# Kernel tuning notes

Hardware: AMD Instinct MI355X
Metric: run time of the kernel (lower is better)

Reference implementation:

```python
import jax, jax.numpy as jnp
import numpy as np

D_MODEL = 768
N_HEAD = 12
HEAD_DIM = D_MODEL // N_HEAD
D_FF = 4 * D_MODEL
EPS = 1e-5


def setup_inputs() -> dict:
    key = jax.random.key(0)
    ks = jax.random.split(key, 12)
    B, S = 4, 1024
    s = 0.02
    return {
        "x": jax.random.normal(ks[0], (B, S, D_MODEL), jnp.float32),
        "ln1_g": jnp.ones((D_MODEL,), jnp.float32),
        "ln1_b": jnp.zeros((D_MODEL,), jnp.float32),
        "ln2_g": jnp.ones((D_MODEL,), jnp.float32),
        "ln2_b": jnp.zeros((D_MODEL,), jnp.float32),
        "w_attn": jax.random.normal(ks[1], (D_MODEL, 3 * D_MODEL), jnp.float32) * s,
        "b_attn": jnp.zeros((3 * D_MODEL,), jnp.float32),
        "w_proj": jax.random.normal(ks[2], (D_MODEL, D_MODEL), jnp.float32) * s,
        "b_proj": jnp.zeros((D_MODEL,), jnp.float32),
        "w_fc": jax.random.normal(ks[3], (D_MODEL, D_FF), jnp.float32) * s,
        "b_fc": jnp.zeros((D_FF,), jnp.float32),
        "w_mlp_proj": jax.random.normal(ks[4], (D_FF, D_MODEL), jnp.float32) * s,
        "b_mlp_proj": jnpp.zeros((D_MODEL,), jnp.float32) if False else jnp.zeros((D_MODEL,), jnp.float32),
    }


def layer_norm(x, g, b):
    mu = jnp.mean(x, axis=-1, keepdims=True)
    var = jnp.mean(jnp.square(x - mu), axis=-1, keepdims=True)
    return (x - mu) * jax.lax.rsqrt(var + EPS) * g + b


def attention(x, w_attn, b_attn, w_proj, b_proj):
    B, S, _ = x.shape
    qkv = x @ w_attn + b_attn                      # [B,S,3D]
    q, k, v = jnp.split(qkv, 3, axis=-1)
    def heads(t):
        return t.reshape(B, S, N_HEAD, HEAD_DIM).transpose(0, 2, 1, 3)  # [B,H,S,hd]
    q, k, v = heads(q), heads(k), heads(v)
    scale = HEAD_DIM ** (-0.5)
    att = jnp.einsum("bhqd,bhkd->bhqk", q, k) * scale
    # additive causal mask: strictly-upper triangle gets -1e9 (matches TF source)
    mask = 1.0 - jnp.tril(jnp.ones((S, S), att.dtype))
    att = att + mask * (-1e9)
    att = jax.nn.softmax(att, axis=-1)
    y = jnp.einsum("bhqk,bhkd->bhqd", att, v)
    y = y.transpose(0, 2, 1, 3).reshape(B, S, D_MODEL)
    return y @ w_proj + b_proj


def mlp(x, w_fc, b_fc, w_mlp_proj, b_mlp_proj):
    h = jax.nn.gelu(x @ w_fc + b_fc, approximate=True)
    return h @ w_mlp_proj + b_mlp_proj


def reference(x, ln1_g, ln1_b, ln2_g, ln2_b, w_attn, b_attn, w_proj, b_proj,
              w_fc, b_fc, w_mlp_proj, b_mlp_proj):
    x = x + attention(layer_norm(x, ln1_g, ln1_b), w_attn, b_attn, w_proj, b_proj)
    x = x + mlp(layer_norm(x, ln2_g, ln2_b), w_fc, b_fc, w_mlp_proj, b_mlp_proj)
    return x
```

## Files before the change

### kernel.cpp

```cpp
#include <hip/hip_runtime.h>

typedef unsigned short u16;
typedef short bf8_t __attribute__((ext_vector_type(8)));
typedef float f32x4 __attribute__((ext_vector_type(4)));

__device__ __forceinline__ u16 f2bf(float f) {
  unsigned u = __builtin_bit_cast(unsigned, f);
  unsigned r = (u + 0x7fffu + ((u >> 16) & 1u)) >> 16;
  return (u16)r;
}

__device__ __forceinline__ void gld16(const void* g, void* l) {
  __builtin_amdgcn_global_load_lds((const __attribute__((address_space(1))) unsigned int*)g,
                                   (__attribute__((address_space(3))) unsigned int*)l, 16, 0, 0);
}

#define MFMA(a, b, c) __builtin_amdgcn_mfma_f32_16x16x32_bf16((a), (b), (c), 0, 0, 0)

__global__ void wtrans_kernel(const float* __restrict__ W, u16* __restrict__ WT, int K, int N) {
  __shared__ float tile[32][33];
  const int n0 = blockIdx.x << 5, k0 = blockIdx.y << 5;
  const int tx = threadIdx.x, ty = threadIdx.y;
#pragma unroll
  for (int i = 0; i < 4; i++) {
    const int r = ty + (i << 3);
    tile[r][tx] = W[(size_t)(k0 + r) * N + n0 + tx];
  }
  __syncthreads();
#pragma unroll
  for (int i = 0; i < 4; i++) {
    const int r = ty + (i << 3);
    WT[(size_t)(n0 + r) * K + k0 + tx] = f2bf(tile[tx][r]);
  }
}

__global__ void ln_kernel(const float* __restrict__ x, const float* __restrict__ g,
                          const float* __restrict__ bb, u16* __restrict__ o) {
  const int row = blockIdx.x, t = threadIdx.x;
  const float* xr = x + (size_t)row * 768;
  float v[3];
#pragma unroll
  for (int i = 0; i < 3; i++) v[i] = xr[t + (i << 8)];
  float s = v[0] + v[1] + v[2];
#pragma unroll
  for (int off = 1; off < 64; off <<= 1) s += __shfl_xor(s, off, 64);
  __shared__ float red[4];
  const int w = t >> 6;
  if ((t & 63) == 0) red[w] = s;
  __syncthreads();
  const float mu = (red[0] + red[1] + red[2] + red[3]) * (1.f / 768.f);
  float q = 0.f;
#pragma unroll
  for (int i = 0; i < 3; i++) {
    v[i] -= mu;
    q += v[i] * v[i];
  }
#pragma unroll
  for (int off = 1; off < 64; off <<= 1) q += __shfl_xor(q, off, 64);
  __syncthreads();
  if ((t & 63) == 0) red[w] = q;
  __syncthreads();
  const float var = (red[0] + red[1] + red[2] + red[3]) * (1.f / 768.f);
  const float rs = rsqrtf(var + 1e-5f);
#pragma unroll
  for (int i = 0; i < 3; i++) {
    const int idx = t + (i << 8);
    o[(size_t)row * 768 + idx] = f2bf(v[i] * rs * g[idx] + bb[idx]);
  }
}

template <int EPI>
__global__ void gemm_kernel(const u16* __restrict__ A, const u16* __restrict__ BT,
                            const float* __restrict__ bias, const float* __restrict__ res,
                            void* __restrict__ outp, int M, int N, int K, int kLen) {
  __shared__ __align__(16) u16 As[2][128 * 32];
  __shared__ __align__(16) u16 Bs[2][128 * 32];
  const int m0 = blockIdx.y << 7, n0 = blockIdx.x << 7;
  const int kOff = blockIdx.z * kLen;
  const int tid = threadIdx.x, lane = tid & 63, w = tid >> 6;
  const int wr = w >> 1, wc = w & 1;
  const int l16 = lane & 15, kg = lane >> 4;
  f32x4 acc[4][4];
  const f32x4 fz = {0.f, 0.f, 0.f, 0.f};
#pragma unroll
  for (int i = 0; i < 4; i++)
#pragma unroll
    for (int j = 0; j < 4; j++) acc[i][j] = fz;

  const int c1 = (w << 6) + lane;
  const int r1 = c1 >> 2, ko1 = (c1 & 3) << 3;
  const int c2 = c1 + 256;
  const int r2 = c2 >> 2, ko2 = (c2 & 3) << 3;
  const int lb1 = (c1 - lane) * 8, lb2 = (c2 - lane) * 8;

  auto stage = [&](int buf, int kt) {
    const int k0 = kOff + (kt << 5);
    gld16(A + (size_t)(m0 + r1) * K + k0 + ko1, As[buf] + lb1);
    gld16(A + (size_t)(m0 + r2) * K + k0 + ko2, As[buf] + lb2);
    gld16(BT + (size_t)(n0 + r1) * K + k0 + ko1, Bs[buf] + lb1);
    gld16(BT + (size_t)(n0 + r2) * K + k0 + ko2, Bs[buf] + lb2);
  };

  const int nkt = kLen >> 5;
  stage(0, 0);
  for (int kt = 0; kt < nkt; kt++) {
    const int cur = kt & 1;
    __syncthreads();
    if (kt + 1 < nkt) stage(cur ^ 1, kt + 1);
    bf8_t af[4], bfr[4];
#pragma unroll
    for (int mf = 0; mf < 4; mf++)
      af[mf] = *(const bf8_t*)&As[cur][((wr << 6) + (mf << 4) + l16) * 32 + (kg << 3)];
#pragma unroll
    for (int nf = 0; nf < 4; nf++)
      bfr[nf] = *(const bf8_t*)&Bs[cur][((wc << 6) + (nf << 4) + l16) * 32 + (kg << 3)];
#pragma unroll
    for (int mf = 0; mf < 4; mf++)
#pragma unroll
      for (int nf = 0; nf < 4; nf++) acc[mf][nf] = MFMA(af[mf], bfr[nf], acc[mf][nf]);
  }
  float* pout = (float*)outp + (size_t)blockIdx.z * M * N;
#pragma unroll
  for (int mf = 0; mf < 4; mf++) {
#pragma unroll
    for (int nf = 0; nf < 4; nf++) {
      const int col = n0 + (wc << 6) + (nf << 4) + l16;
      const float bv = (EPI == 3) ? 0.f : bias[col];
#pragma unroll
      for (int j = 0; j < 4; j++) {
        const int row = m0 + (wr << 6) + (mf << 4) + (kg << 2) + j;
        float v = acc[mf][nf][j] + bv;
        if constexpr (EPI == 0) {
          ((u16*)outp)[(size_t)row * N + col] = f2bf(v);
        } else if constexpr (EPI == 1) {
          const float u = 0.7978845608f * (v + 0.044715f * v * v * v);
          const float e = __expf(2.f * u);
          const float th = 1.f - 2.f / (e + 1.f);
          ((u16*)outp)[(size_t)row * N + col] = f2bf(0.5f * v * (1.f + th));
        } else if constexpr (EPI == 2) {
          v += res[(size_t)row * N + col];
          ((float*)outp)[(size_t)row * N + col] = v;
        } else {
          pout[(size_t)row * N + col] = v;
        }
      }
    }
  }
}

__global__ void reduce_kernel(const float* __restrict__ parts, const float* __restrict__ bias,
                              const float* __restrict__ res, float* __restrict__ out, int ns) {
  const int row = blockIdx.x, col = threadIdx.x << 2;
  const size_t base = (size_t)row * 768 + col;
  f32x4 a = *(const f32x4*)(parts + base);
  for (int s = 1; s < ns; s++) a += *(const f32x4*)(parts + (size_t)s * 4096 * 768 + base);
  const f32x4 bv = *(const f32x4*)(bias + col);
  const f32x4 rv = *(const f32x4*)(res + base);
  *(f32x4*)(out + base) = a + bv + rv;
}

__global__ void attn_kernel(const u16* __restrict__ qkv, u16* __restrict__ y) {
  __shared__ __align__(16) u16 Qs[64 * 64];
  __shared__ __align__(16) u16 Ks[2][64 * 64];
  __shared__ __align__(16) u16 Vt[2][64 * 64];
  __shared__ __align__(16) u16 Ps[4][16 * 72];
  const int qt = (int)gridDim.x - 1 - (int)blockIdx.x;
  const int bh = blockIdx.y;
  const int b = bh / 12, h = bh - b * 12;
  const size_t brow = (size_t)b << 10;
  const int q0 = qt << 6;
  const int tid = threadIdx.x, lane = tid & 63, w = tid >> 6;
  const int l16 = lane & 15, kg = lane >> 4;

  const int c1 = tid, c2 = tid + 256;
  const int row1 = c1 >> 3, cc1 = c1 & 7;
  const int row2 = c2 >> 3, cc2 = c2 & 7;
  const int sw1 = ((cc1 ^ (row1 & 7)) << 3);
  const int sw2 = ((cc2 ^ (row2 & 7)) << 3);
  const int sg1 = ((cc1 & 1) << 2) | (cc1 & 2) | ((cc1 >> 2) & 1);
  const int sg2 = ((cc2 & 1) << 2) | (cc2 & 2) | ((cc2 >> 2) & 1);
  const int vcol1 = row1 ^ (sg1 << 3), d01 = cc1 << 3;
  const int vcol2 = row2 ^ (sg2 << 3), d02 = cc2 << 3;

  const int cbQ = h << 6, cbK = 768 + (h << 6), cbV = 1536 + (h << 6);

  gld16(qkv + (brow + q0 + row1) * 2304 + cbQ + sw1, Qs + (size_t)(c1 - lane) * 8);
  gld16(qkv + (brow + q0 + row2) * 2304 + cbQ + sw2, Qs + (size_t)(c2 - lane) * 8);
  gld16(qkv + (brow + row1) * 2304 + cbK + sw1, Ks[0] + (size_t)(c1 - lane) * 8);
  gld16(qkv + (brow + row2) * 2304 + cbK + sw2, Ks[0] + (size_t)(c2 - lane) * 8);
  bf8_t v1 = *(const bf8_t*)(qkv + (brow + row1) * 2304 + cbV + (cc1 << 3));
  bf8_t v2 = *(const bf8_t*)(qkv + (brow + row2) * 2304 + cbV + (cc2 << 3));

  bf8_t qf[2];
  f32x4 oacc[4];
  const f32x4 fz = {0.f, 0.f, 0.f, 0.f};
#pragma unroll
  for (int dg = 0; dg < 4; dg++) oacc[dg] = fz;
  float mrun[4], lrun[4];
#pragma unroll
  for (int j = 0; j < 4; j++) {
    mrun[j] = -1e30f;
    lrun[j] = 0.f;
  }

  for (int kt = 0; kt <= qt; kt++) {
    const int cur = kt & 1;
    u16* Vc = Vt[cur];
#pragma unroll
    for (int i = 0; i < 8; i++) Vc[(d01 + i) * 64 + vcol1] = (u16)v1[i];
#pragma unroll
    for (int i = 0; i < 8; i++) Vc[(d02 + i) * 64 + vcol2] = (u16)v2[i];
    __syncthreads();

    if (kt == 0) {
      const int qrow = (w << 4) + l16;
#pragma unroll
      for (int hd = 0; hd < 2; hd++) {
        const int ch = (kg + (hd << 2)) ^ (qrow & 7);
        qf[hd] = *(const bf8_t*)&Qs[qrow * 64 + (ch << 3)];
      }
    }
    if (kt < qt) {
      const int nr = (kt + 1) << 6;
      gld16(qkv + (brow + nr + row1) * 2304 + cbK + sw1, Ks[cur ^ 1] + (size_t)(c1 - lane) * 8);
      gld16(qkv + (brow + nr + row2) * 2304 + cbK + sw2, Ks[cur ^ 1] + (size_t)(c2 - lane) * 8);
      v1 = *(const bf8_t*)(qkv + (brow + nr + row1) * 2304 + cbV + (cc1 << 3));
      v2 = *(const bf8_t*)(qkv + (brow + nr + row2) * 2304 + cbV + (cc2 << 3));
    }

    const u16* Kc = Ks[cur];
    float sv[4][4];
#pragma unroll
    for (int g = 0; g < 4; g++) {
      f32x4 z = fz;
      const int key = (g << 4) + l16;
#pragma unroll
      for (int hd = 0; hd < 2; hd++) {
        const int ch = (kg + (hd << 2)) ^ (key & 7);
        const bf8_t kf = *(const bf8_t*)&Kc[key * 64 + (ch << 3)];
        z = MFMA(qf[hd], kf, z);
      }
      const int gkey = (kt << 6) + key;
#pragma unroll
      for (int j = 0; j < 4; j++) {
        const int grow = q0 + (w << 4) + (kg << 2) + j;
        sv[g][j] = (gkey <= grow) ? z[j] * 0.125f : -1e30f;
      }
    }
    float tm[4];
#pragma unroll
    for (int j = 0; j < 4; j++)
      tm[j] = fmaxf(fmaxf(sv[0][j], sv[1][j]), fmaxf(sv[2][j], sv[3][j]));
#pragma unroll
    for (int o = 1; o < 16; o <<= 1)
#pragma unroll
      for (int j = 0; j < 4; j++) tm[j] = fmaxf(tm[j], __shfl_xor(tm[j], o, 64));
    float corr[4], tsum[4];
#pragma unroll
    for (int j = 0; j < 4; j++) {
      const float mn = fmaxf(mrun[j], tm[j]);
      corr[j] = __expf(mrun[j] - mn);
      mrun[j] = mn;
      tsum[j] = 0.f;
    }
#pragma unroll
    for (int g = 0; g < 4; g++)
#pragma unroll
      for (int j = 0; j < 4; j++) {
        const float p = __expf(sv[g][j] - mrun[j]);
        sv[g][j] = p;
        tsum[j] += p;
      }
#pragma unroll
    for (int o = 1; o < 16; o <<= 1)
#pragma unroll
      for (int j = 0; j < 4; j++) tsum[j] += __shfl_xor(tsum[j], o, 64);
#pragma unroll
    for (int j = 0; j < 4; j++) lrun[j] = lrun[j] * corr[j] + tsum[j];
#pragma unroll
    for (int dg = 0; dg < 4; dg++)
#pragma unroll
      for (int j = 0; j < 4; j++) oacc[dg][j] *= corr[j];
#pragma unroll
    for (int g = 0; g < 4; g++)
#pragma unroll
      for (int j = 0; j < 4; j++)
        Ps[w][((kg << 2) + j) * 72 + (g << 4) + l16] = f2bf(sv[g][j]);
    bf8_t pf[2];
#pragma unroll
    for (int kh = 0; kh < 2; kh++)
      pf[kh] = *(const bf8_t*)&Ps[w][l16 * 72 + (kg << 3) + (kh << 5)];
#pragma unroll
    for (int dg = 0; dg < 4; dg++) {
      const int sgr = (((l16 >> 3) & 1) << 2) | ((dg & 1) << 1) | (dg >> 1);
      const int d = (dg << 4) + l16;
#pragma unroll
      for (int kh = 0; kh < 2; kh++) {
        const bf8_t vf = *(const bf8_t*)&Vc[d * 64 + ((((kh << 2) + kg) ^ sgr) << 3)];
        oacc[dg] = MFMA(pf[kh], vf, oacc[dg]);
      }
    }
  }
  float inv[4];
#pragma unroll
  for (int j = 0; j < 4; j++) inv[j] = 1.f / lrun[j];
#pragma unroll
  for (int dg = 0; dg < 4; dg++)
#pragma unroll
    for (int j = 0; j < 4; j++) {
      const size_t grow = brow + q0 + (w << 4) + (kg << 2) + j;
      y[grow * 768 + (h << 6) + (dg << 4) + l16] = f2bf(oacc[dg][j] * inv[j]);
    }
}

extern "C" void kernel_launch(void* const* d_in, const int* in_sizes, int n_in,
                              void* d_out, int out_size, void* d_ws, size_t ws_size,
                              hipStream_t stream) {
  const float* x = (const float*)d_in[0];
  const float* ln1_g = (const float*)d_in[1];
  const float* ln1_b = (const float*)d_in[2];
  const float* ln2_g = (const float*)d_in[3];
  const float* ln2_b = (const float*)d_in[4];
  const float* w_attn = (const float*)d_in[5];
  const float* b_attn = (const float*)d_in[6];
  const float* w_proj = (const float*)d_in[7];
  const float* b_proj = (const float*)d_in[8];
  const float* w_fc = (const float*)d_in[9];
  const float* b_fc = (const float*)d_in[10];
  const float* w_mlp = (const float*)d_in[11];
  const float* b_mlp = (const float*)d_in[12];
  float* out = (float*)d_out;

  char* ws = (char*)d_ws;
  u16* wqkvT = (u16*)(ws + 0);
  u16* wprojT = (u16*)(ws + 3538944);
  u16* wfcT = (u16*)(ws + 4718592);
  u16* wmlpT = (u16*)(ws + 9437184);
  u16* xn = (u16*)(ws + 14155776);
  u16* qkv = (u16*)(ws + 20447232);
  u16* hbuf = (u16*)(ws + 20447232);
  u16* yb = (u16*)(ws + 45613056);
  float* x1 = (float*)(ws + 51904512);
  float* parts = (float*)(ws + 64487424);

  const size_t PSZ = (size_t)4096 * 768 * 4;
  const int nsMlp = (ws_size >= 64487424 + 4 * PSZ) ? 4 : (ws_size >= 64487424 + 2 * PSZ ? 2 : 1);
  const int nsProj = (ws_size >= 64487424 + 2 * PSZ) ? 2 : 1;

  const dim3 wtb(32, 8);
  wtrans_kernel<<<dim3(2304 / 32, 768 / 32), wtb, 0, stream>>>(w_attn, wqkvT, 768, 2304);
  wtrans_kernel<<<dim3(768 / 32, 768 / 32), wtb, 0, stream>>>(w_proj, wprojT, 768, 768);
  wtrans_kernel<<<dim3(3072 / 32, 768 / 32), wtb, 0, stream>>>(w_fc, wfcT, 768, 3072);
  wtrans_kernel<<<dim3(768 / 32, 3072 / 32), wtb, 0, stream>>>(w_mlp, wmlpT, 3072, 768);

  ln_kernel<<<4096, 256, 0, stream>>>(x, ln1_g, ln1_b, xn);
  gemm_kernel<0><<<dim3(18, 32), 256, 0, stream>>>(xn, wqkvT, b_attn, nullptr, qkv,
                                                   4096, 2304, 768, 768);
  attn_kernel<<<dim3(16, 48), 256, 0, stream>>>(qkv, yb);

  if (nsProj == 2) {
    gemm_kernel<3><<<dim3(6, 32, 2), 256, 0, stream>>>(yb, wprojT, nullptr, nullptr, parts,
                                                       4096, 768, 768, 384);
    reduce_kernel<<<4096, 192, 0, stream>>>(parts, b_proj, x, x1, 2);
  } else {
    gemm_kernel<2><<<dim3(6, 32), 256, 0, stream>>>(yb, wprojT, b_proj, x, x1,
                                                    4096, 768, 768, 768);
  }

  ln_kernel<<<4096, 256, 0, stream>>>(x1, ln2_g, ln2_b, xn);
  gemm_kernel<1><<<dim3(24, 32), 256, 0, stream>>>(xn, wfcT, b_fc, nullptr, hbuf,
                                                   4096, 3072, 768, 768);

  if (nsMlp > 1) {
    gemm_kernel<3><<<dim3(6, 32, nsMlp), 256, 0, stream>>>(hbuf, wmlpT, nullptr, nullptr, parts,
                                                           4096, 768, 3072, 3072 / nsMlp);
    reduce_kernel<<<4096, 192, 0, stream>>>(parts, b_mlp, x1, out, nsMlp);
  } else {
    gemm_kernel<2><<<dim3(6, 32), 256, 0, stream>>>(hbuf, wmlpT, b_mlp, x1, out,
                                                    4096, 768, 3072, 3072);
  }
}
```

Baseline: 213.9 us.

## Pre-transpose V and load attention K/V fragments directly from global into registers

A new kernel transposes the V part of the QKV buffer into a per-head [d, seq] layout in workspace. The attention kernel then drops its LDS staging for Q, K and V and the per-tile syncthreads, loading MFMA operand fragments straight from global memory. K fragments are double-buffered in registers across a two-step unrolled loop. The aim is to remove LDS traffic, the scattered V transpose writes and block barriers, at the cost of an extra launch, extra global traffic for vT, more registers, and uncoalesced per-lane global loads that lean on cache reuse across waves.

```diff
diff --git a/kernel.cpp b/kernel.cpp
--- a/kernel.cpp
+++ b/kernel.cpp
@@ -31,6 +31,24 @@
   for (int i = 0; i < 4; i++) {
     const int r = ty + (i << 3);
     WT[(size_t)(n0 + r) * K + k0 + tx] = f2bf(tile[tx][r]);
+  }
+}
+
+__global__ void vtrans_kernel(const u16* __restrict__ qkv, u16* __restrict__ vT) {
+  __shared__ u16 tile[32][33];
+  const int c0 = blockIdx.x << 5, r0 = blockIdx.y << 5;
+  const int tx = threadIdx.x, ty = threadIdx.y;
+#pragma unroll
+  for (int i = 0; i < 4; i++) {
+    const int r = ty + (i << 3);
+    tile[r][tx] = qkv[(size_t)(r0 + r) * 2304 + 1536 + c0 + tx];
+  }
+  __syncthreads();
+  const int b = r0 >> 10, s0 = r0 & 1023;
+#pragma unroll
+  for (int i = 0; i < 4; i++) {
+    const int c = ty + (i << 3);
+    vT[((size_t)b * 768 + c0 + c) * 1024 + s0 + tx] = tile[tx][c];
   }
 }
 
@@ -159,39 +177,25 @@
   *(f32x4*)(out + base) = a + bv + rv;
 }
 
-__global__ void attn_kernel(const u16* __restrict__ qkv, u16* __restrict__ y) {
-  __shared__ __align__(16) u16 Qs[64 * 64];
-  __shared__ __align__(16) u16 Ks[2][64 * 64];
-  __shared__ __align__(16) u16 Vt[2][64 * 64];
+__global__ void attn_kernel(const u16* __restrict__ qkv, const u16* __restrict__ vT,
+                            u16* __restrict__ y) {
   __shared__ __align__(16) u16 Ps[4][16 * 72];
   const int qt = (int)gridDim.x - 1 - (int)blockIdx.x;
   const int bh = blockIdx.y;
   const int b = bh / 12, h = bh - b * 12;
   const size_t brow = (size_t)b << 10;
-  const int q0 = qt << 6;
   const int tid = threadIdx.x, lane = tid & 63, w = tid >> 6;
   const int l16 = lane & 15, kg = lane >> 4;
-
-  const int c1 = tid, c2 = tid + 256;
-  const int row1 = c1 >> 3, cc1 = c1 & 7;
-  const int row2 = c2 >> 3, cc2 = c2 & 7;
-  const int sw1 = ((cc1 ^ (row1 & 7)) << 3);
-  const int sw2 = ((cc2 ^ (row2 & 7)) << 3);
-  const int sg1 = ((cc1 & 1) << 2) | (cc1 & 2) | ((cc1 >> 2) & 1);
-  const int sg2 = ((cc2 & 1) << 2) | (cc2 & 2) | ((cc2 >> 2) & 1);
-  const int vcol1 = row1 ^ (sg1 << 3), d01 = cc1 << 3;
-  const int vcol2 = row2 ^ (sg2 << 3), d02 = cc2 << 3;
-
-  const int cbQ = h << 6, cbK = 768 + (h << 6), cbV = 1536 + (h << 6);
-
-  gld16(qkv + (brow + q0 + row1) * 2304 + cbQ + sw1, Qs + (size_t)(c1 - lane) * 8);
-  gld16(qkv + (brow + q0 + row2) * 2304 + cbQ + sw2, Qs + (size_t)(c2 - lane) * 8);
-  gld16(qkv + (brow + row1) * 2304 + cbK + sw1, Ks[0] + (size_t)(c1 - lane) * 8);
-  gld16(qkv + (brow + row2) * 2304 + cbK + sw2, Ks[0] + (size_t)(c2 - lane) * 8);
-  bf8_t v1 = *(const bf8_t*)(qkv + (brow + row1) * 2304 + cbV + (cc1 << 3));
-  bf8_t v2 = *(const bf8_t*)(qkv + (brow + row2) * 2304 + cbV + (cc2 << 3));
+  const int q0w = (qt << 6) + (w << 4);
+
+  const u16* Qbase = qkv + (brow + q0w + l16) * 2304 + (h << 6) + (kg << 3);
+  const u16* Kbase = qkv + brow * 2304 + 768 + (h << 6) + (kg << 3);
+  const u16* Vbase = vT + ((size_t)(bh << 6) + l16) * 1024 + (kg << 3);
 
   bf8_t qf[2];
+#pragma unroll
+  for (int hd = 0; hd < 2; hd++) qf[hd] = *(const bf8_t*)(Qbase + (hd << 5));
+
   f32x4 oacc[4];
   const f32x4 fz = {0.f, 0.f, 0.f, 0.f};
 #pragma unroll
@@ -203,50 +207,34 @@
     lrun[j] = 0.f;
   }
 
-  for (int kt = 0; kt <= qt; kt++) {
-    const int cur = kt & 1;
-    u16* Vc = Vt[cur];
-#pragma unroll
-    for (int i = 0; i < 8; i++) Vc[(d01 + i) * 64 + vcol1] = (u16)v1[i];
-#pragma unroll
-    for (int i = 0; i < 8; i++) Vc[(d02 + i) * 64 + vcol2] = (u16)v2[i];
-    __syncthreads();
-
-    if (kt == 0) {
-      const int qrow = (w << 4) + l16;
-#pragma unroll
-      for (int hd = 0; hd < 2; hd++) {
-        const int ch = (kg + (hd << 2)) ^ (qrow & 7);
-        qf[hd] = *(const bf8_t*)&Qs[qrow * 64 + (ch << 3)];
-      }
-    }
+  auto body = [&](int kt, bf8_t(&kc)[4][2], bf8_t(&kn)[4][2]) {
     if (kt < qt) {
       const int nr = (kt + 1) << 6;
-      gld16(qkv + (brow + nr + row1) * 2304 + cbK + sw1, Ks[cur ^ 1] + (size_t)(c1 - lane) * 8);
-      gld16(qkv + (brow + nr + row2) * 2304 + cbK + sw2, Ks[cur ^ 1] + (size_t)(c2 - lane) * 8);
-      v1 = *(const bf8_t*)(qkv + (brow + nr + row1) * 2304 + cbV + (cc1 << 3));
-      v2 = *(const bf8_t*)(qkv + (brow + nr + row2) * 2304 + cbV + (cc2 << 3));
-    }
-
-    const u16* Kc = Ks[cur];
+#pragma unroll
+      for (int g = 0; g < 4; g++)
+#pragma unroll
+        for (int hd = 0; hd < 2; hd++)
+          kn[g][hd] = *(const bf8_t*)(Kbase + (size_t)(nr + (g << 4) + l16) * 2304 + (hd << 5));
+    }
     float sv[4][4];
 #pragma unroll
     for (int g = 0; g < 4; g++) {
       f32x4 z = fz;
-      const int key = (g << 4) + l16;
-#pragma unroll
-      for (int hd = 0; hd < 2; hd++) {
-        const int ch = (kg + (hd << 2)) ^ (key & 7);
-        const bf8_t kf = *(const bf8_t*)&Kc[key * 64 + (ch << 3)];
-        z = MFMA(qf[hd], kf, z);
-      }
-      const int gkey = (kt << 6) + key;
+#pragma unroll
+      for (int hd = 0; hd < 2; hd++) z = MFMA(qf[hd], kc[g][hd], z);
+      const int gkey = (kt << 6) + (g << 4) + l16;
 #pragma unroll
       for (int j = 0; j < 4; j++) {
-        const int grow = q0 + (w << 4) + (kg << 2) + j;
+        const int grow = q0w + (kg << 2) + j;
         sv[g][j] = (gkey <= grow) ? z[j] * 0.125f : -1e30f;
       }
     }
+    bf8_t vf[4][2];
+#pragma unroll
+    for (int dg = 0; dg < 4; dg++)
+#pragma unroll
+      for (int kh = 0; kh < 2; kh++)
+        vf[dg][kh] = *(const bf8_t*)(Vbase + ((size_t)dg << 14) + (kt << 6) + (kh << 5));
     float tm[4];
 #pragma unroll
     for (int j = 0; j < 4; j++)
@@ -291,16 +279,22 @@
     for (int kh = 0; kh < 2; kh++)
       pf[kh] = *(const bf8_t*)&Ps[w][l16 * 72 + (kg << 3) + (kh << 5)];
 #pragma unroll
-    for (int dg = 0; dg < 4; dg++) {
-      const int sgr = (((l16 >> 3) & 1) << 2) | ((dg & 1) << 1) | (dg >> 1);
-      const int d = (dg << 4) + l16;
-#pragma unroll
-      for (int kh = 0; kh < 2; kh++) {
-        const bf8_t vf = *(const bf8_t*)&Vc[d * 64 + ((((kh << 2) + kg) ^ sgr) << 3)];
-        oacc[dg] = MFMA(pf[kh], vf, oacc[dg]);
-      }
-    }
-  }
+    for (int dg = 0; dg < 4; dg++)
+#pragma unroll
+      for (int kh = 0; kh < 2; kh++) oacc[dg] = MFMA(pf[kh], vf[dg][kh], oacc[dg]);
+  };
+
+  bf8_t kA[4][2], kB[4][2];
+#pragma unroll
+  for (int g = 0; g < 4; g++)
+#pragma unroll
+    for (int hd = 0; hd < 2; hd++)
+      kA[g][hd] = *(const bf8_t*)(Kbase + (size_t)((g << 4) + l16) * 2304 + (hd << 5));
+  for (int kt = 0; kt <= qt; kt += 2) {
+    body(kt, kA, kB);
+    if (kt + 1 <= qt) body(kt + 1, kB, kA);
+  }
+
   float inv[4];
 #pragma unroll
   for (int j = 0; j < 4; j++) inv[j] = 1.f / lrun[j];
@@ -308,7 +302,7 @@
   for (int dg = 0; dg < 4; dg++)
 #pragma unroll
     for (int j = 0; j < 4; j++) {
-      const size_t grow = brow + q0 + (w << 4) + (kg << 2) + j;
+      const size_t grow = brow + q0w + (kg << 2) + j;
       y[grow * 768 + (h << 6) + (dg << 4) + l16] = f2bf(oacc[dg][j] * inv[j]);
     }
 }
@@ -342,6 +336,7 @@
   u16* yb = (u16*)(ws + 45613056);
   float* x1 = (float*)(ws + 51904512);
   float* parts = (float*)(ws + 64487424);
+  u16* vT = (u16*)(ws + 64487424);
 
   const size_t PSZ = (size_t)4096 * 768 * 4;
   const int nsMlp = (ws_size >= 64487424 + 4 * PSZ) ? 4 : (ws_size >= 64487424 + 2 * PSZ ? 2 : 1);
@@ -356,7 +351,8 @@
   ln_kernel<<<4096, 256, 0, stream>>>(x, ln1_g, ln1_b, xn);
   gemm_kernel<0><<<dim3(18, 32), 256, 0, stream>>>(xn, wqkvT, b_attn, nullptr, qkv,
                                                    4096, 2304, 768, 768);
-  attn_kernel<<<dim3(16, 48), 256, 0, stream>>>(qkv, yb);
+  vtrans_kernel<<<dim3(24, 128), wtb, 0, stream>>>(qkv, vT);
+  attn_kernel<<<dim3(16, 48), 256, 0, stream>>>(qkv, vT, yb);
 
   if (nsProj == 2) {
     gemm_kernel<3><<<dim3(6, 32, 2), 256, 0, stream>>>(yb, wprojT, nullptr, nullptr, parts,
```

After: 294.0 us. 37.5% more time.

## Split causal attention KV range into chunks with a separate combine kernel

Applied to the files above, without the earlier changes.

The attention kernel can now split each query tile's causal key range into chunks of up to four key tiles, launching 40 blocks per batch-head instead of 16. This evens out the load imbalance between short and long causal rows. Each chunk writes a bf16 partial output plus its running max and sum, and a new combine kernel merges them with log-sum-exp weights. Q fragments are now read straight from global memory instead of through LDS, and the kernel gets a launch-bounds hint. The cost is an extra launch, extra global traffic for the partials, and a small accuracy loss from storing partial outputs in bf16.

```diff
diff --git a/kernel.cpp b/kernel.cpp
--- a/kernel.cpp
+++ b/kernel.cpp
@@ -8,6 +8,11 @@
   unsigned u = __builtin_bit_cast(unsigned, f);
   unsigned r = (u + 0x7fffu + ((u >> 16) & 1u)) >> 16;
   return (u16)r;
+}
+
+__device__ __forceinline__ float b2f(u16 v) {
+  unsigned u = ((unsigned)v) << 16;
+  return __builtin_bit_cast(float, u);
 }
 
 __device__ __forceinline__ void gld16(const void* g, void* l) {
@@ -159,12 +164,33 @@
   *(f32x4*)(out + base) = a + bv + rv;
 }
 
-__global__ void attn_kernel(const u16* __restrict__ qkv, u16* __restrict__ y) {
-  __shared__ __align__(16) u16 Qs[64 * 64];
+template <bool SPLIT>
+__global__ __launch_bounds__(256, 3) void attn_kernel(const u16* __restrict__ qkv,
+                                                      u16* __restrict__ part_o,
+                                                      float* __restrict__ partML,
+                                                      u16* __restrict__ y) {
   __shared__ __align__(16) u16 Ks[2][64 * 64];
   __shared__ __align__(16) u16 Vt[2][64 * 64];
   __shared__ __align__(16) u16 Ps[4][16 * 72];
-  const int qt = (int)gridDim.x - 1 - (int)blockIdx.x;
+  int qt, c, t0, t1;
+  if constexpr (SPLIT) {
+    const int cid = 39 - (int)blockIdx.x;
+    int g = 0, base = 0;
+    while (cid >= base + 4 * (g + 1)) {
+      base += 4 * (g + 1);
+      g++;
+    }
+    const int r = cid - base;
+    qt = (g << 2) + r / (g + 1);
+    c = r % (g + 1);
+    t0 = c << 2;
+    t1 = min(t0 + 4, qt + 1);
+  } else {
+    qt = (int)gridDim.x - 1 - (int)blockIdx.x;
+    c = 0;
+    t0 = 0;
+    t1 = qt + 1;
+  }
   const int bh = blockIdx.y;
   const int b = bh / 12, h = bh - b * 12;
   const size_t brow = (size_t)b << 10;
@@ -182,16 +208,17 @@
   const int vcol1 = row1 ^ (sg1 << 3), d01 = cc1 << 3;
   const int vcol2 = row2 ^ (sg2 << 3), d02 = cc2 << 3;
 
-  const int cbQ = h << 6, cbK = 768 + (h << 6), cbV = 1536 + (h << 6);
-
-  gld16(qkv + (brow + q0 + row1) * 2304 + cbQ + sw1, Qs + (size_t)(c1 - lane) * 8);
-  gld16(qkv + (brow + q0 + row2) * 2304 + cbQ + sw2, Qs + (size_t)(c2 - lane) * 8);
-  gld16(qkv + (brow + row1) * 2304 + cbK + sw1, Ks[0] + (size_t)(c1 - lane) * 8);
-  gld16(qkv + (brow + row2) * 2304 + cbK + sw2, Ks[0] + (size_t)(c2 - lane) * 8);
-  bf8_t v1 = *(const bf8_t*)(qkv + (brow + row1) * 2304 + cbV + (cc1 << 3));
-  bf8_t v2 = *(const bf8_t*)(qkv + (brow + row2) * 2304 + cbV + (cc2 << 3));
-
-  bf8_t qf[2];
+  const int cbK = 768 + (h << 6), cbV = 1536 + (h << 6);
+
+  const u16* Qbase = qkv + (brow + q0 + (w << 4) + l16) * 2304 + (h << 6) + (kg << 3);
+  const bf8_t qf0 = *(const bf8_t*)(Qbase);
+  const bf8_t qf1 = *(const bf8_t*)(Qbase + 32);
+
+  gld16(qkv + (brow + (t0 << 6) + row1) * 2304 + cbK + sw1, Ks[t0 & 1] + (size_t)(c1 - lane) * 8);
+  gld16(qkv + (brow + (t0 << 6) + row2) * 2304 + cbK + sw2, Ks[t0 & 1] + (size_t)(c2 - lane) * 8);
+  bf8_t v1 = *(const bf8_t*)(qkv + (brow + (t0 << 6) + row1) * 2304 + cbV + (cc1 << 3));
+  bf8_t v2 = *(const bf8_t*)(qkv + (brow + (t0 << 6) + row2) * 2304 + cbV + (cc2 << 3));
+
   f32x4 oacc[4];
   const f32x4 fz = {0.f, 0.f, 0.f, 0.f};
 #pragma unroll
@@ -203,7 +230,7 @@
     lrun[j] = 0.f;
   }
 
-  for (int kt = 0; kt <= qt; kt++) {
+  for (int kt = t0; kt < t1; kt++) {
     const int cur = kt & 1;
     u16* Vc = Vt[cur];
 #pragma unroll
@@ -212,15 +239,7 @@
     for (int i = 0; i < 8; i++) Vc[(d02 + i) * 64 + vcol2] = (u16)v2[i];
     __syncthreads();
 
-    if (kt == 0) {
-      const int qrow = (w << 4) + l16;
-#pragma unroll
-      for (int hd = 0; hd < 2; hd++) {
-        const int ch = (kg + (hd << 2)) ^ (qrow & 7);
-        qf[hd] = *(const bf8_t*)&Qs[qrow * 64 + (ch << 3)];
-      }
-    }
-    if (kt < qt) {
+    if (kt + 1 < t1) {
       const int nr = (kt + 1) << 6;
       gld16(qkv + (brow + nr + row1) * 2304 + cbK + sw1, Ks[cur ^ 1] + (size_t)(c1 - lane) * 8);
       gld16(qkv + (brow + nr + row2) * 2304 + cbK + sw2, Ks[cur ^ 1] + (size_t)(c2 - lane) * 8);
@@ -238,7 +257,17 @@
       for (int hd = 0; hd < 2; hd++) {
         const int ch = (kg + (hd << 2)) ^ (key & 7);
         const bf8_t kf = *(const bf8_t*)&Kc[key * 64 + (ch << 3)];
-        z = MFMA(qf[hd], kf, z);
+        z = MFMA(qf0, kf, z);
+        if (hd == 0) {
+        }
+      }
+      {
+        const int ch0 = kg ^ (key & 7);
+        const int ch1 = (kg + 4) ^ (key & 7);
+        f32x4 zz = fz;
+        zz = MFMA(qf0, *(const bf8_t*)&Kc[key * 64 + (ch0 << 3)], zz);
+        zz = MFMA(qf1, *(const bf8_t*)&Kc[key * 64 + (ch1 << 3)], zz);
+        z = zz;
       }
       const int gkey = (kt << 6) + key;
 #pragma unroll
@@ -286,31 +315,96 @@
 #pragma unroll
       for (int j = 0; j < 4; j++)
         Ps[w][((kg << 2) + j) * 72 + (g << 4) + l16] = f2bf(sv[g][j]);
-    bf8_t pf[2];
-#pragma unroll
-    for (int kh = 0; kh < 2; kh++)
-      pf[kh] = *(const bf8_t*)&Ps[w][l16 * 72 + (kg << 3) + (kh << 5)];
+    const bf8_t pf0 = *(const bf8_t*)&Ps[w][l16 * 72 + (kg << 3)];
+    const bf8_t pf1 = *(const bf8_t*)&Ps[w][l16 * 72 + (kg << 3) + 32];
 #pragma unroll
     for (int dg = 0; dg < 4; dg++) {
       const int sgr = (((l16 >> 3) & 1) << 2) | ((dg & 1) << 1) | (dg >> 1);
       const int d = (dg << 4) + l16;
-#pragma unroll
-      for (int kh = 0; kh < 2; kh++) {
-        const bf8_t vf = *(const bf8_t*)&Vc[d * 64 + ((((kh << 2) + kg) ^ sgr) << 3)];
-        oacc[dg] = MFMA(pf[kh], vf, oacc[dg]);
-      }
-    }
-  }
+      oacc[dg] = MFMA(pf0, *(const bf8_t*)&Vc[d * 64 + ((kg ^ sgr) << 3)], oacc[dg]);
+      oacc[dg] = MFMA(pf1, *(const bf8_t*)&Vc[d * 64 + (((4 + kg) ^ sgr) << 3)], oacc[dg]);
+    }
+  }
+
   float inv[4];
 #pragma unroll
   for (int j = 0; j < 4; j++) inv[j] = 1.f / lrun[j];
-#pragma unroll
-  for (int dg = 0; dg < 4; dg++)
-#pragma unroll
-    for (int j = 0; j < 4; j++) {
-      const size_t grow = brow + q0 + (w << 4) + (kg << 2) + j;
-      y[grow * 768 + (h << 6) + (dg << 4) + l16] = f2bf(oacc[dg][j] * inv[j]);
-    }
+  if constexpr (SPLIT) {
+    const int slot = (((bh << 4) + qt) << 2) + c;
+    u16* po = part_o + (size_t)slot * 4096;
+#pragma unroll
+    for (int dg = 0; dg < 4; dg++)
+#pragma unroll
+      for (int j = 0; j < 4; j++)
+        po[((w << 4) + (kg << 2) + j) * 64 + (dg << 4) + l16] = f2bf(oacc[dg][j] * inv[j]);
+    if (l16 == 0) {
+#pragma unroll
+      for (int j = 0; j < 4; j++) {
+        const int rr = (w << 4) + (kg << 2) + j;
+        partML[(size_t)slot * 128 + rr * 2] = mrun[j];
+        partML[(size_t)slot * 128 + rr * 2 + 1] = lrun[j];
+      }
+    }
+  } else {
+#pragma unroll
+    for (int dg = 0; dg < 4; dg++)
+#pragma unroll
+      for (int j = 0; j < 4; j++) {
+        const size_t grow = brow + q0 + (w << 4) + (kg << 2) + j;
+        y[grow * 768 + (h << 6) + (dg << 4) + l16] = f2bf(oacc[dg][j] * inv[j]);
+      }
+  }
+}
+
+__global__ void attn_combine(const u16* __restrict__ part_o, const float* __restrict__ partML,
+                             u16* __restrict__ y) {
+  const int qt = blockIdx.x, bh = blockIdx.y;
+  const int nc = (qt >> 2) + 1;
+  const int tid = threadIdx.x;
+  const int r = tid >> 2, cg = tid & 3;
+  const int b = bh / 12, h = bh - b * 12;
+  const int slot0 = ((bh << 4) + qt) << 2;
+  float mv0 = -1e30f, mv1 = -1e30f, mv2 = -1e30f, mv3 = -1e30f;
+  float lv0 = 0.f, lv1 = 0.f, lv2 = 0.f, lv3 = 0.f;
+  mv0 = partML[(size_t)(slot0 + 0) * 128 + r * 2];
+  lv0 = partML[(size_t)(slot0 + 0) * 128 + r * 2 + 1];
+  if (nc > 1) {
+    mv1 = partML[(size_t)(slot0 + 1) * 128 + r * 2];
+    lv1 = partML[(size_t)(slot0 + 1) * 128 + r * 2 + 1];
+  }
+  if (nc > 2) {
+    mv2 = partML[(size_t)(slot0 + 2) * 128 + r * 2];
+    lv2 = partML[(size_t)(slot0 + 2) * 128 + r * 2 + 1];
+  }
+  if (nc > 3) {
+    mv3 = partML[(size_t)(slot0 + 3) * 128 + r * 2];
+    lv3 = partML[(size_t)(slot0 + 3) * 128 + r * 2 + 1];
+  }
+  const float M = fmaxf(fmaxf(mv0, mv1), fmaxf(mv2, mv3));
+  const float w0 = __expf(mv0 - M) * lv0;
+  const float w1 = (nc > 1) ? __expf(mv1 - M) * lv1 : 0.f;
+  const float w2 = (nc > 2) ? __expf(mv2 - M) * lv2 : 0.f;
+  const float w3 = (nc > 3) ? __expf(mv3 - M) * lv3 : 0.f;
+  const float invL = 1.f / (w0 + w1 + w2 + w3);
+  float acc[16];
+#pragma unroll
+  for (int i = 0; i < 16; i++) acc[i] = 0.f;
+#pragma unroll
+  for (int cc = 0; cc < 4; cc++) {
+    if (cc < nc) {
+      const float wv = (cc == 0) ? w0 : (cc == 1) ? w1 : (cc == 2) ? w2 : w3;
+      const bf8_t* op = (const bf8_t*)(part_o + (size_t)(slot0 + cc) * 4096 + r * 64 + (cg << 4));
+      const bf8_t o0 = op[0], o1 = op[1];
+#pragma unroll
+      for (int i = 0; i < 8; i++) {
+        acc[i] += wv * b2f((u16)o0[i]);
+        acc[8 + i] += wv * b2f((u16)o1[i]);
+      }
+    }
+  }
+  u16* yp = y + ((size_t)(b << 10) + (qt << 6) + r) * 768 + (h << 6) + (cg << 4);
+#pragma unroll
+  for (int i = 0; i < 16; i++) yp[i] = f2bf(acc[i] * invL);
 }
 
 extern "C" void kernel_launch(void* const* d_in, const int* in_sizes, int n_in,
@@ -342,10 +436,13 @@
   u16* yb = (u16*)(ws + 45613056);
   float* x1 = (float*)(ws + 51904512);
   float* parts = (float*)(ws + 64487424);
+  u16* part_o = (u16*)(ws + 64487424);
+  float* partML = (float*)(ws + 89653248);
 
   const size_t PSZ = (size_t)4096 * 768 * 4;
   const int nsMlp = (ws_size >= 64487424 + 4 * PSZ) ? 4 : (ws_size >= 64487424 + 2 * PSZ ? 2 : 1);
   const int nsProj = (ws_size >= 64487424 + 2 * PSZ) ? 2 : 1;
+  const bool useSplit = ws_size >= 91226112;
 
   const dim3 wtb(32, 8);
   wtrans_kernel<<<dim3(2304 / 32, 768 / 32), wtb, 0, stream>>>(w_attn, wqkvT, 768, 2304);
@@ -356,7 +453,12 @@
   ln_kernel<<<4096, 256, 0, stream>>>(x, ln1_g, ln1_b, xn);
   gemm_kernel<0><<<dim3(18, 32), 256, 0, stream>>>(xn, wqkvT, b_attn, nullptr, qkv,
                                                    4096, 2304, 768, 768);
-  attn_kernel<<<dim3(16, 48), 256, 0, stream>>>(qkv, yb);
+  if (useSplit) {
+    attn_kernel<true><<<dim3(40, 48), 256, 0, stream>>>(qkv, part_o, partML, yb);
+    attn_combine<<<dim3(16, 48), 256, 0, stream>>>(part_o, partML, yb);
+  } else {
+    attn_kernel<false><<<dim3(16, 48), 256, 0, stream>>>(qkv, part_o, partML, yb);
+  }
 
   if (nsProj == 2) {
     gemm_kernel<3><<<dim3(6, 32, 2), 256, 0, stream>>>(yb, wprojT, nullptr, nullptr, parts,
```

Measured after the change: 204.2 us. 1.05x faster.
